# Kernel optimization log

Measured on AMD Instinct MI355X. Metric: run time of the kernel, lower is better.

## Reference

```python
import jax, jax.numpy as jnp
import numpy as np

N_NODES = 100000
N_EDGES = 1600000
N_GRAPHS = 100
HEADS = 8
OUT_CH = 16
IN_FEAT = 128
EPS = 1e-5
NEG_SLOPE = 0.2


def setup_inputs() -> dict:
    key = jax.random.key(0)
    ks = jax.random.split(key, 8)
    x = jax.random.normal(ks[0], (N_NODES, IN_FEAT), dtype=jnp.float32)
    edge_index = jax.random.randint(ks[1], (2, N_EDGES), 0, N_NODES, dtype=jnp.int64)
    batch = jnp.sort(jax.random.randint(ks[2], (N_NODES,), 0, N_GRAPHS, dtype=jnp.int64))
    bn_gamma = jnp.ones((IN_FEAT,), jnp.float32)
    bn_beta = jnp.zeros((IN_FEAT,), jnp.float32)
    W = jax.random.normal(ks[3], (IN_FEAT, HEADS * OUT_CH), dtype=jnp.float32) * (1.0 / np.sqrt(IN_FEAT))
    att_src = jax.random.normal(ks[4], (HEADS, OUT_CH), dtype=jnp.float32) * 0.1
    att_dst = jax.random.normal(ks[5], (HEADS, OUT_CH), dtype=jnp.float32) * 0.1
    bias = jnp.zeros((OUT_CH,), jnp.float32)
    return {"x": x, "edge_index": edge_index, "batch": batch,
            "bn_gamma": bn_gamma, "bn_beta": bn_beta, "W": W,
            "att_src": att_src, "att_dst": att_dst, "bias": bias}


def reference(x, edge_index, batch, bn_gamma, bn_beta, W, att_src, att_dst, bias):
    N = x.shape[0]
    # BatchNorm1d (training mode: batch statistics, biased variance)
    mean = jnp.mean(x, axis=0)
    var = jnp.var(x, axis=0)
    xn = (x - mean) * jax.lax.rsqrt(var + EPS) * bn_gamma + bn_beta

    # GATConv (heads=HEADS, concat=False), with self-loops as in PyG default
    loop = jnp.arange(N, dtype=edge_index.dtype)
    src = jnp.concatenate([edge_index[0], loop])  # [Et]
    dst = jnp.concatenate([edge_index[1], loop])  # [Et]

    h = (xn @ W).reshape(N, HEADS, OUT_CH)  # [N,H,C]
    a_src = jnp.einsum('nhc,hc->nh', h, att_src)  # [N,H]
    a_dst = jnp.einsum('nhc,hc->nh', h, att_dst)  # [N,H]

    e = a_src[src] + a_dst[dst]  # [Et,H]
    e = jnp.where(e > 0, e, NEG_SLOPE * e)  # leaky_relu(0.2)
    # scatter-softmax over destination node (self-loops => every segment nonempty)
    m = jax.ops.segment_max(e, dst, num_segments=N)  # [N,H]
    e = jnp.exp(e - m[dst])
    s = jax.ops.segment_sum(e, dst, num_segments=N)  # [N,H]
    alpha = e / s[dst]  # [Et,H]

    msg = alpha[:, :, None] * h[src]  # [Et,H,C]
    out = jax.ops.segment_sum(msg, dst, num_segments=N)  # [N,H,C]
    out = out.mean(axis=1) + bias  # concat=False -> head mean, [N,C]

    out = jax.nn.elu(out)

    # global_mean_pool over graph ids
    sums = jax.ops.segment_sum(out, batch, num_segments=N_GRAPHS)  # [G,C]
    cnt = jax.ops.segment_sum(jnp.ones((N,), out.dtype), batch, num_segments=N_GRAPHS)
    return sums / jnp.maximum(cnt, 1.0)[:, None]
```

## Files before the change

kernel.cpp:

```cpp
#include <hip/hip_runtime.h>
#include <hip/hip_bf16.h>
#include <hip/hip_fp16.h>


#define N_NODES 100000
#define N_EDGE  1600000
#define N_ET    1700000
#define N_G     100
#define HEADS   8
#define OUTC    16
#define EPS     1e-5f
#define NEG     0.2f
#define NB_BUCKETS 196
#define BCAP    9472
#define EPB     3321

typedef unsigned int uint;
typedef unsigned short ushort;
typedef float f32x2 __attribute__((ext_vector_type(2)));
typedef float f32x4 __attribute__((ext_vector_type(4)));
typedef __bf16 bf16x8 __attribute__((ext_vector_type(8)));

__device__ __forceinline__ float bf2f_lo(uint u){ union{uint i; float f;} c; c.i = u << 16; return c.f; }
__device__ __forceinline__ float bf2f_hi(uint u){ union{uint i; float f;} c; c.i = u & 0xffff0000u; return c.f; }
__device__ __forceinline__ float bf2f(ushort u){ union{uint i; float f;} c; c.i = ((uint)u) << 16; return c.f; }
__device__ __forceinline__ float scrub(float v){ return (v == v) ? v : 0.f; }

__device__ __forceinline__ ushort f2bf(float f){
  union{float ff; uint u;} c; c.ff = f;
  uint u = c.u;
  if ((u & 0x7fffffffu) > 0x7f800000u) u = 0;
  return (ushort)((u + 0x7fffu + ((u >> 16) & 1u)) >> 16);
}
__device__ __forceinline__ ushort bfsan(ushort u){
  return ((ushort)(u & 0x7fffu) > (ushort)0x7f80u) ? (ushort)0 : u;
}

__device__ __forceinline__ float ldf(const void* p, int i, int f32){
  return f32 ? ((const float*)p)[i] : bf2f(((const ushort*)p)[i]);
}
__device__ __forceinline__ int ldid(const int* p, int flat, int is64){
  return is64 ? p[2 * flat] : p[flat];
}

__global__ __launch_bounds__(256) void k_front(const void* __restrict__ xraw,
                                               float* __restrict__ stats,
                                               const int* __restrict__ ei,
                                               int* __restrict__ bcnt,
                                               uint* __restrict__ pairBuf){
  int t = threadIdx.x;
  if (blockIdx.x < 512){
    __shared__ int cdet;
    __shared__ float red[4][256];
    if (t == 0) cdet = 0;
    __syncthreads();
    { uint w = ((const uint*)xraw)[t]; uint el = (w >> 7) & 0xffu;
      if (el != 0 && (el < 110 || el > 140)) atomicAdd(&cdet, 1); }
    __syncthreads();
    int f32 = cdet > 64;
    int c = t & 63;
    int c0 = c * 2;
    float s0 = 0.f, s1 = 0.f, q0 = 0.f, q1 = 0.f;
    if (f32){
      const float2* x2 = (const float2*)xraw;
      for (int r = blockIdx.x * 4 + (t >> 6); r < N_NODES; r += 2048){
        float2 v = x2[r * 64 + c];
        float f0 = scrub(v.x), f1 = scrub(v.y);
        s0 += f0; q0 += f0 * f0;
        s1 += f1; q1 += f1 * f1;
      }
    } else {
      const uint* x2 = (const uint*)xraw;
      for (int r = blockIdx.x * 4 + (t >> 6); r < N_NODES; r += 2048){
        uint v = x2[r * 64 + c];
        float f0 = scrub(bf2f_lo(v)), f1 = scrub(bf2f_hi(v));
        s0 += f0; q0 += f0 * f0;
        s1 += f1; q1 += f1 * f1;
      }
    }
    red[0][t] = s0; red[1][t] = q0; red[2][t] = s1; red[3][t] = q1;
    __syncthreads();
    if (t < 64){
      s0 = red[0][t] + red[0][t+64] + red[0][t+128] + red[0][t+192];
      q0 = red[1][t] + red[1][t+64] + red[1][t+128] + red[1][t+192];
      s1 = red[2][t] + red[2][t+64] + red[2][t+128] + red[2][t+192];
      q1 = red[3][t] + red[3][t+64] + red[3][t+128] + red[3][t+192];
      atomicAdd(&stats[c0],       s0);
      atomicAdd(&stats[c0+1],     s1);
      atomicAdd(&stats[128+c0],   q0);
      atomicAdd(&stats[128+c0+1], q1);
    }
  } else {
    __shared__ int hist[NB_BUCKETS];
    __shared__ int base[NB_BUCKETS];
    __shared__ int cdet2;
    int bid = blockIdx.x - 512;
    if (t == 0) cdet2 = 0;
    for (int i = t; i < NB_BUCKETS; i += 256) hist[i] = 0;
    __syncthreads();
    if (t < 128){ if (ei[2 * t + 1] != 0) atomicAdd(&cdet2, 1); }
    __syncthreads();
    int is64 = cdet2 < 32;
    int e0 = bid * EPB, e1 = min(e0 + EPB, N_ET);
    for (int e = e0 + t; e < e1; e += 256){
      int d = (e < N_EDGE) ? ldid(ei, N_EDGE + e, is64) : (e - N_EDGE);
      uint b = (uint)d >> 9; if (b >= NB_BUCKETS) b = NB_BUCKETS - 1;
      atomicAdd(&hist[b], 1);
    }
    __syncthreads();
    for (int i = t; i < NB_BUCKETS; i += 256){
      int c = hist[i];
      base[i] = c ? atomicAdd(&bcnt[i], c) : 0;
      hist[i] = 0;
    }
    __syncthreads();
    for (int e = e0 + t; e < e1; e += 256){
      int s, d;
      if (e < N_EDGE){ s = ldid(ei, e, is64); d = ldid(ei, N_EDGE + e, is64); }
      else { s = d = e - N_EDGE; }
      uint b = (uint)d >> 9; if (b >= NB_BUCKETS) b = NB_BUCKETS - 1;
      int pos = base[b] + atomicAdd(&hist[b], 1);
      if ((uint)pos < BCAP) pairBuf[(size_t)b * BCAP + pos] = ((uint)s << 9) | ((uint)d & 511u);
    }
  }
}

__global__ __launch_bounds__(128) void k_prep(const float* __restrict__ stats,
                                              const void* __restrict__ gamma,
                                              const void* __restrict__ beta,
                                              const void* __restrict__ W,
                                              const uint* __restrict__ x32,
                                              const int* __restrict__ b32,
                                              ushort* __restrict__ Wpb,
                                              float* __restrict__ bp,
                                              int* __restrict__ flags){
  __shared__ int cnt[2];
  __shared__ float scl8[8], shf8[8];
  int t = threadIdx.x, bid = blockIdx.x;
  if (t < 2) cnt[t] = 0;
  __syncthreads();
  { uint w = x32[t];       uint el = (w >> 7) & 0xffu;
    if (el != 0 && (el < 110 || el > 140)) atomicAdd(&cnt[0], 1); }
  { uint w = x32[t + 128]; uint el = (w >> 7) & 0xffu;
    if (el != 0 && (el < 110 || el > 140)) atomicAdd(&cnt[0], 1); }
  if (bid == 0){ if (b32[98001 + 2 * t] != 0) atomicAdd(&cnt[1], 1); }
  __syncthreads();
  int f32 = cnt[0] > 64;
  if (bid == 0 && t == 0){
    flags[0] = f32;
    flags[1] = 0;
    flags[2] = cnt[1] < 32;
    flags[3] = 0;
  }
  if (t < 8){
    int c = bid * 8 + t;
    float mean = scrub(stats[c] * (1.0f / N_NODES));
    float var  = stats[128 + c] * (1.0f / N_NODES) - mean * mean;
    if (!(var > 0.f)) var = 0.f;
    float sc = scrub(ldf(gamma, c, f32)) * rsqrtf(var + EPS);
    sc = scrub(sc);
    scl8[t] = sc;
    shf8[t] = scrub(scrub(ldf(beta, c, f32)) - mean * sc);
  }
  __syncthreads();
  float bacc = 0.f;
#pragma unroll
  for (int j = 0; j < 8; j++){
    int c = bid * 8 + j;
    float w = scrub(ldf(W, c * 128 + t, f32));
    Wpb[t * 128 + (c & 7) + (((c >> 3) ^ (t & 15)) << 3)] = f2bf(scl8[j] * w);
    bacc += shf8[j] * w;
  }
  atomicAdd(&bp[t], scrub(bacc));
}

__global__ __launch_bounds__(256) void k_gemm(const void* __restrict__ xraw,
                                              const ushort* __restrict__ Wpb,
                                              const float* __restrict__ bp,
                                              const void* __restrict__ att_src,
                                              const void* __restrict__ att_dst,
                                              const int* __restrict__ flags,
                                              unsigned char* __restrict__ h8,
                                              __half* __restrict__ a_src16,
                                              __half* __restrict__ a_dst16){
  int f32 = flags[0];
  __shared__ __align__(16) char smem[33792];
  __shared__ float sSL[128], sDL[128], bpL[128];
  int t = threadIdx.x;
  int wv = t >> 6, l = t & 63;
  int row0 = blockIdx.x * 64;
  if (t < 128){
    sSL[t] = scrub(ldf(att_src, t, f32));
    sDL[t] = scrub(ldf(att_dst, t, f32));
    bpL[t] = bp[t];
  }
  {
    const uint4* wsrc = (const uint4*)Wpb;
    uint4* wdst = (uint4*)smem;
#pragma unroll
    for (int i = 0; i < 8; i++)
      wdst[i * 256 + t] = wsrc[i * 256 + t];
  }
  __syncthreads();
  ushort* BsT = (ushort*)smem;

  f32x4 acc[8];
#pragma unroll
  for (int ct = 0; ct < 8; ct++) acc[ct] = (f32x4){0.f, 0.f, 0.f, 0.f};
  int arow = row0 + wv * 16 + (l & 15);
  int cr = min(arow, N_NODES - 1);
  int kg = (l >> 4) * 8;
  union AB { uint4 q; bf16x8 v; ushort u[8]; };
#pragma unroll
  for (int kc = 0; kc < 4; kc++){
    AB a;
    if (f32){
      const float* xr = (const float*)xraw + (size_t)cr * 128 + kc * 32 + kg;
      float4 p0 = *(const float4*)xr;
      float4 p1 = *(const float4*)(xr + 4);
      a.u[0] = f2bf(p0.x); a.u[1] = f2bf(p0.y); a.u[2] = f2bf(p0.z); a.u[3] = f2bf(p0.w);
      a.u[4] = f2bf(p1.x); a.u[5] = f2bf(p1.y); a.u[6] = f2bf(p1.z); a.u[7] = f2bf(p1.w);
    } else {
      const ushort* xr = (const ushort*)xraw + (size_t)cr * 128 + kc * 32 + kg;
      a.q = *(const uint4*)xr;
#pragma unroll
      for (int j = 0; j < 8; j++) a.u[j] = bfsan(a.u[j]);
    }
#pragma unroll
    for (int ct = 0; ct < 8; ct++){
      int c = ct * 16 + (l & 15);
      int kb = kc * 4 + (l >> 4);
      AB bfr;
      bfr.q = *(const uint4*)(BsT + c * 128 + ((kb ^ (c & 15)) << 3));
      acc[ct] = __builtin_amdgcn_mfma_f32_16x16x32_bf16(a.v, bfr.v, acc[ct], 0, 0, 0);
    }
  }
  __syncthreads();
  float* Cs = (float*)smem;
#pragma unroll
  for (int ct = 0; ct < 8; ct++){
#pragma unroll
    for (int ri = 0; ri < 4; ri++)
      Cs[(wv * 16 + (l >> 4) * 4 + ri) * 132 + ct * 16 + (l & 15)] = acc[ct][ri];
  }
  __syncthreads();
  int row = t >> 2, cg = (t & 3) * 32;
  int r = row0 + row;
  if (r < N_NODES){
    float o[32];
#pragma unroll
    for (int i = 0; i < 8; i++){
      float4 v = *(const float4*)(Cs + row * 132 + cg + i * 4);
      o[i*4+0] = v.x; o[i*4+1] = v.y; o[i*4+2] = v.z; o[i*4+3] = v.w;
    }
#pragma unroll
    for (int j = 0; j < 32; j++){
      float v = scrub(o[j] + bpL[cg + j]);
      o[j] = fminf(fmaxf(v, -448.f), 448.f);
    }
    uint w[8];
#pragma unroll
    for (int i = 0; i < 8; i++){
      uint ww = __builtin_amdgcn_cvt_pk_fp8_f32(o[i*4+0], o[i*4+1], 0, false);
      w[i] = __builtin_amdgcn_cvt_pk_fp8_f32(o[i*4+2], o[i*4+3], (int)ww, true);
    }
    unsigned char* po = h8 + (size_t)r * 128 + cg;
    *(uint4*)po        = make_uint4(w[0], w[1], w[2], w[3]);
    *(uint4*)(po + 16) = make_uint4(w[4], w[5], w[6], w[7]);
    float s0 = 0.f, s1 = 0.f, d0 = 0.f, d1 = 0.f;
#pragma unroll
    for (int j = 0; j < 16; j++){
      s0 += o[j]      * sSL[cg + j];      d0 += o[j]      * sDL[cg + j];
      s1 += o[16 + j] * sSL[cg + 16 + j]; d1 += o[16 + j] * sDL[cg + 16 + j];
    }
    int hA = (t & 3) * 2;
    *(__half2*)(a_src16 + (size_t)r * 8 + hA) = __floats2half2_rn(scrub(s0), scrub(s1));
    *(__half2*)(a_dst16 + (size_t)r * 8 + hA) = __floats2half2_rn(scrub(d0), scrub(d1));
  }
}

__global__ __launch_bounds__(1024) void k_binC(const uint* __restrict__ pairBuf,
                                               const int* __restrict__ bcnt,
                                               int* __restrict__ offsets,
                                               int* __restrict__ csr){
  int b = blockIdx.x, t = threadIdx.x;
  __shared__ int sscan[256];
  __shared__ int degL[512];
  __shared__ int offL[512];
  __shared__ int curL[512];
  if (t < 256) sscan[t] = (t < NB_BUCKETS) ? min(bcnt[t], BCAP) : 0;
  if (t < 512) degL[t] = 0;
  __syncthreads();
  for (int off = 1; off < 256; off <<= 1){
    int add = (t < 256 && t >= off) ? sscan[t - off] : 0;
    __syncthreads();
    if (t < 256) sscan[t] += add;
    __syncthreads();
  }
  int gbase = (b == 0) ? 0 : sscan[b - 1];
  if (b == NB_BUCKETS - 1 && t == 0) offsets[N_NODES] = sscan[NB_BUCKETS - 1];
  int cnt = min(bcnt[b], BCAP);
  const uint* run = pairBuf + (size_t)b * BCAP;
  for (int i = t; i < cnt; i += 1024)
    atomicAdd(&degL[run[i] & 511u], 1);
  __syncthreads();
  int v = (t < 512) ? degL[t] : 0;
  if (t < 512) offL[t] = v;
  __syncthreads();
  for (int off = 1; off < 512; off <<= 1){
    int add = (t < 512 && t >= off) ? offL[t - off] : 0;
    __syncthreads();
    if (t < 512) offL[t] += add;
    __syncthreads();
  }
  if (t < 512){
    int excl = offL[t] - v;
    int node = (b << 9) + t;
    if (node < N_NODES) offsets[node] = gbase + excl;
    offL[t] = excl;
    curL[t] = 0;
  }
  __syncthreads();
  for (int i = t; i < cnt; i += 1024){
    uint e = run[i];
    int dl = e & 511u;
    int s  = e >> 9;
    int pos = atomicAdd(&curL[dl], 1);
    csr[gbase + offL[dl] + pos] = s;
  }
}

__global__ __launch_bounds__(256) void k_msg(const int* __restrict__ offsets, const int* __restrict__ csr,
                                             const __half* __restrict__ a_src16, const __half* __restrict__ a_dst16,
                                             const uint* __restrict__ h32, const void* __restrict__ bias,
                                             const int* __restrict__ flags,
                                             float* __restrict__ out_n){
  int f32 = flags[0];
  int t = threadIdx.x;
  int wv = t >> 6, lane = t & 63;
  int half = lane >> 5, li = lane & 31;
  int myh = li >> 2;
  int n = blockIdx.x * 4 + wv;
  int start = offsets[n], end = offsets[n + 1];
  float ad = __half2float(a_dst16[(size_t)n * 8 + myh]);
  const ushort* as16 = (const ushort*)a_src16;
  float acc0 = 0.f, acc1 = 0.f, acc2 = 0.f, acc3 = 0.f, den = 0.f;

#define PAIR(AA, HH)                                                  \
  { float e = __half2float(*(__half*)&(AA)) + ad;                     \
    e = fmaxf(e, NEG * e);                                            \
    float p = __expf(fminf(e, 30.f));                                 \
    f32x2 lo = __builtin_amdgcn_cvt_pk_f32_fp8((int)(HH), false);     \
    f32x2 hi = __builtin_amdgcn_cvt_pk_f32_fp8((int)(HH), true);      \
    den += p; acc0 += p * lo[0]; acc1 += p * lo[1];                   \
    acc2 += p * hi[0]; acc3 += p * hi[1]; }

  for (int base = start; base < end; base += 64){
    int cnt = min(64, end - base);
    int sreg = csr[min(base + lane, N_ET - 1)];
    int npair = cnt >> 1;
    int jj = 0;
    for (; jj + 4 <= npair; jj += 4){
      int i0 = 2 * jj + half;
      int s0 = __shfl(sreg, i0);
      int s1 = __shfl(sreg, i0 + 2);
      int s2 = __shfl(sreg, i0 + 4);
      int s3 = __shfl(sreg, i0 + 6);
      uint h0 = h32[(uint)s0 * 32u + li];
      uint h1 = h32[(uint)s1 * 32u + li];
      uint h2 = h32[(uint)s2 * 32u + li];
      uint h3 = h32[(uint)s3 * 32u + li];
      ushort a0 = as16[(uint)s0 * 8u + myh];
      ushort a1 = as16[(uint)s1 * 8u + myh];
      ushort a2 = as16[(uint)s2 * 8u + myh];
      ushort a3 = as16[(uint)s3 * 8u + myh];
      __builtin_amdgcn_sched_barrier(0);
      PAIR(a0, h0) PAIR(a1, h1) PAIR(a2, h2) PAIR(a3, h3)
    }
    for (; jj < npair; jj++){
      int s0 = __shfl(sreg, 2 * jj + half);
      uint h0 = h32[(uint)s0 * 32u + li];
      ushort a0 = as16[(uint)s0 * 8u + myh];
      PAIR(a0, h0)
    }
    if (cnt & 1){
      int sl = __shfl(sreg, cnt - 1);
      uint hh = h32[(uint)sl * 32u + li];
      ushort aa = as16[(uint)sl * 8u + myh];
      float e = __half2float(*(__half*)&aa) + ad;
      e = fmaxf(e, NEG * e);
      float p = __expf(fminf(e, 30.f));
      p = half ? 0.f : p;
      f32x2 lo = __builtin_amdgcn_cvt_pk_f32_fp8((int)hh, false);
      f32x2 hi = __builtin_amdgcn_cvt_pk_f32_fp8((int)hh, true);
      den += p; acc0 += p * lo[0]; acc1 += p * lo[1];
      acc2 += p * hi[0]; acc3 += p * hi[1];
    }
  }
#undef PAIR

  den  += __shfl_xor(den, 32);
  acc0 += __shfl_xor(acc0, 32);
  acc1 += __shfl_xor(acc1, 32);
  acc2 += __shfl_xor(acc2, 32);
  acc3 += __shfl_xor(acc3, 32);
  float inv = (den > 0.f) ? (1.0f / den) : 0.f;
  float v0 = acc0 * inv, v1 = acc1 * inv, v2 = acc2 * inv, v3 = acc3 * inv;
  v0 += __shfl_xor(v0, 4);  v1 += __shfl_xor(v1, 4);  v2 += __shfl_xor(v2, 4);  v3 += __shfl_xor(v3, 4);
  v0 += __shfl_xor(v0, 8);  v1 += __shfl_xor(v1, 8);  v2 += __shfl_xor(v2, 8);  v3 += __shfl_xor(v3, 8);
  v0 += __shfl_xor(v0, 16); v1 += __shfl_xor(v1, 16); v2 += __shfl_xor(v2, 16); v3 += __shfl_xor(v3, 16);
  if (lane < 4){
    int c0 = lane * 4;
    float o0 = v0 * 0.125f + scrub(ldf(bias, c0 + 0, f32));
    float o1 = v1 * 0.125f + scrub(ldf(bias, c0 + 1, f32));
    float o2 = v2 * 0.125f + scrub(ldf(bias, c0 + 2, f32));
    float o3 = v3 * 0.125f + scrub(ldf(bias, c0 + 3, f32));
    o0 = o0 > 0.f ? o0 : (__expf(o0) - 1.0f);
    o1 = o1 > 0.f ? o1 : (__expf(o1) - 1.0f);
    o2 = o2 > 0.f ? o2 : (__expf(o2) - 1.0f);
    o3 = o3 > 0.f ? o3 : (__expf(o3) - 1.0f);
    float4* po = (float4*)(out_n + (size_t)n * 16 + c0);
    *po = make_float4(scrub(o0), scrub(o1), scrub(o2), scrub(o3));
  }
}

__global__ __launch_bounds__(256) void k_pool(const float* __restrict__ out_n,
                                              const int* __restrict__ batch,
                                              const int* __restrict__ flags,
                                              float* __restrict__ out){
  int b64 = flags[2];
  int g = blockIdx.x;
  int t = threadIdx.x;
  int c = t & 15, rg = t >> 4;
  int lo = 0, hi = N_NODES;
  while (lo < hi){ int m = (lo + hi) >> 1; if (ldid(batch, m, b64) < g) lo = m + 1; else hi = m; }
  int lo2 = lo, hi2 = N_NODES;
  while (lo2 < hi2){ int m = (lo2 + hi2) >> 1; if (ldid(batch, m, b64) < g + 1) lo2 = m + 1; else hi2 = m; }
  float acc = 0.f;
  for (int r = lo + rg; r < lo2; r += 16)
    acc += out_n[(size_t)r * 16 + c];
  __shared__ float red[16][17];
  red[rg][c] = acc;
  __syncthreads();
  if (t < 16){
    float v = 0.f;
#pragma unroll
    for (int i = 0; i < 16; i++) v += red[i][t];
    float cntf = (float)(lo2 - lo);
    out[g * 16 + t] = scrub(v / fmaxf(cntf, 1.0f));
  }
}

extern "C" void kernel_launch(void* const* d_in, const int* in_sizes, int n_in,
                              void* d_out, int out_size, void* d_ws, size_t ws_size,
                              hipStream_t stream){
  (void)in_sizes; (void)n_in; (void)out_size; (void)ws_size;
  const void* x     = d_in[0];
  const int*  ei    = (const int*)d_in[1];
  const int*  batch = (const int*)d_in[2];
  const void* gamma = d_in[3];
  const void* beta  = d_in[4];
  const void* W     = d_in[5];
  const void* att_s = d_in[6];
  const void* att_d = d_in[7];
  const void* bias  = d_in[8];

  char* ws = (char*)d_ws;
  size_t off = 0;
  auto alloc = [&](size_t b){ size_t r = off; off += (b + 255) & ~(size_t)255; return r; };
  int*    flags   = (int*)(ws + alloc(4 * 4));
  float*  stats   = (float*)(ws + alloc(256 * 4));
  float*  bp      = (float*)(ws + alloc(128 * 4));
  int*    bcnt    = (int*)(ws + alloc(NB_BUCKETS * 4));
  size_t  zero_end = off;
  ushort* Wpb     = (ushort*)(ws + alloc(16384 * 2));
  int*    offsets = (int*)(ws + alloc((size_t)(N_NODES + 1) * 4));
  __half* a_src16 = (__half*)(ws + alloc((size_t)N_NODES * 8 * 2));
  __half* a_dst16 = (__half*)(ws + alloc((size_t)N_NODES * 8 * 2));
  size_t  pb_bytes = (size_t)NB_BUCKETS * BCAP * 4;
  size_t  on_bytes = (size_t)N_NODES * 16 * 4;
  char*   pb_region = ws + alloc(pb_bytes > on_bytes ? pb_bytes : on_bytes);
  uint*   pairBuf = (uint*)pb_region;
  float*  out_n   = (float*)pb_region;
  unsigned char* h8 = (unsigned char*)(ws + alloc((size_t)N_NODES * 128));
  int*    csr     = (int*)(ws + alloc((size_t)N_ET * 4));

  hipMemsetAsync(ws, 0, zero_end, stream);

  k_front<<<1024, 256, 0, stream>>>(x, stats, ei, bcnt, pairBuf);
  k_prep<<<16, 128, 0, stream>>>(stats, gamma, beta, W, (const uint*)x, batch, Wpb, bp, flags);
  k_gemm<<<(N_NODES + 63) / 64, 256, 0, stream>>>(x, Wpb, bp, att_s, att_d, flags, h8, a_src16, a_dst16);
  k_binC<<<NB_BUCKETS, 1024, 0, stream>>>(pairBuf, bcnt, offsets, csr);
  k_msg<<<N_NODES / 4, 256, 0, stream>>>(offsets, csr, a_src16, a_dst16, (const uint*)h8, bias, flags, out_n);
  k_pool<<<N_G, 256, 0, stream>>>(out_n, batch, flags, (float*)d_out);
}
```

Baseline: 279.0 us.

## Fuse prep and CSR build kernels, use finer buckets, cache edges in LDS

Merges the BN/weight prep kernel and the per-bucket CSR build into one launch (k_mid). Destination buckets shrink from 512 to 256 nodes, giving more, smaller bucket blocks. The edge-binning blocks now read each edge once and keep the packed pair and bucket id in shared memory for the scatter pass, instead of re-reading edge_index. The split between stats blocks and binning blocks is rebalanced. This cuts one kernel launch and some global reads, at the cost of more LDS per block and 512-thread blocks in the fused kernel.

```diff
diff --git a/kernel.cpp b/kernel.cpp
--- a/kernel.cpp
+++ b/kernel.cpp
@@ -11,9 +11,11 @@
 #define OUTC    16
 #define EPS     1e-5f
 #define NEG     0.2f
-#define NB_BUCKETS 196
-#define BCAP    9472
-#define EPB     3321
+#define NB_BUCKETS 391
+#define BCAP    4864
+#define BNB     384
+#define ABB     640
+#define EPB     2657
 
 typedef unsigned int uint;
 typedef unsigned short ushort;
@@ -49,7 +51,7 @@
                                                int* __restrict__ bcnt,
                                                uint* __restrict__ pairBuf){
   int t = threadIdx.x;
-  if (blockIdx.x < 512){
+  if (blockIdx.x < BNB){
     __shared__ int cdet;
     __shared__ float red[4][256];
     if (t == 0) cdet = 0;
@@ -63,7 +65,7 @@
     float s0 = 0.f, s1 = 0.f, q0 = 0.f, q1 = 0.f;
     if (f32){
       const float2* x2 = (const float2*)xraw;
-      for (int r = blockIdx.x * 4 + (t >> 6); r < N_NODES; r += 2048){
+      for (int r = blockIdx.x * 4 + (t >> 6); r < N_NODES; r += BNB * 4){
         float2 v = x2[r * 64 + c];
         float f0 = scrub(v.x), f1 = scrub(v.y);
         s0 += f0; q0 += f0 * f0;
@@ -71,7 +73,7 @@
       }
     } else {
       const uint* x2 = (const uint*)xraw;
-      for (int r = blockIdx.x * 4 + (t >> 6); r < N_NODES; r += 2048){
+      for (int r = blockIdx.x * 4 + (t >> 6); r < N_NODES; r += BNB * 4){
         uint v = x2[r * 64 + c];
         float f0 = scrub(bf2f_lo(v)), f1 = scrub(bf2f_hi(v));
         s0 += f0; q0 += f0 * f0;
@@ -93,8 +95,10 @@
   } else {
     __shared__ int hist[NB_BUCKETS];
     __shared__ int base[NB_BUCKETS];
+    __shared__ uint   ebuf[EPB];
+    __shared__ ushort bktL[EPB];
     __shared__ int cdet2;
-    int bid = blockIdx.x - 512;
+    int bid = blockIdx.x - BNB;
     if (t == 0) cdet2 = 0;
     for (int i = t; i < NB_BUCKETS; i += 256) hist[i] = 0;
     __syncthreads();
@@ -103,9 +107,15 @@
     int is64 = cdet2 < 32;
     int e0 = bid * EPB, e1 = min(e0 + EPB, N_ET);
     for (int e = e0 + t; e < e1; e += 256){
-      int d = (e < N_EDGE) ? ldid(ei, N_EDGE + e, is64) : (e - N_EDGE);
-      uint b = (uint)d >> 9; if (b >= NB_BUCKETS) b = NB_BUCKETS - 1;
+      int s, d;
+      if (e < N_EDGE){ s = ldid(ei, e, is64); d = ldid(ei, N_EDGE + e, is64); }
+      else { s = d = e - N_EDGE; }
+      uint dd = (uint)d; if (dd >= N_NODES) dd = 0;
+      uint ss = (uint)s; if (ss >= N_NODES) ss = 0;
+      uint b = dd >> 8;
       atomicAdd(&hist[b], 1);
+      ebuf[e - e0] = (ss << 8) | (dd & 255u);
+      bktL[e - e0] = (ushort)b;
     }
     __syncthreads();
     for (int i = t; i < NB_BUCKETS; i += 256){
@@ -114,64 +124,119 @@
       hist[i] = 0;
     }
     __syncthreads();
-    for (int e = e0 + t; e < e1; e += 256){
-      int s, d;
-      if (e < N_EDGE){ s = ldid(ei, e, is64); d = ldid(ei, N_EDGE + e, is64); }
-      else { s = d = e - N_EDGE; }
-      uint b = (uint)d >> 9; if (b >= NB_BUCKETS) b = NB_BUCKETS - 1;
+    int n_e = e1 - e0;
+    for (int j = t; j < n_e; j += 256){
+      uint b = bktL[j];
       int pos = base[b] + atomicAdd(&hist[b], 1);
-      if ((uint)pos < BCAP) pairBuf[(size_t)b * BCAP + pos] = ((uint)s << 9) | ((uint)d & 511u);
-    }
-  }
-}
-
-__global__ __launch_bounds__(128) void k_prep(const float* __restrict__ stats,
-                                              const void* __restrict__ gamma,
-                                              const void* __restrict__ beta,
-                                              const void* __restrict__ W,
-                                              const uint* __restrict__ x32,
-                                              const int* __restrict__ b32,
-                                              ushort* __restrict__ Wpb,
-                                              float* __restrict__ bp,
-                                              int* __restrict__ flags){
-  __shared__ int cnt[2];
-  __shared__ float scl8[8], shf8[8];
-  int t = threadIdx.x, bid = blockIdx.x;
-  if (t < 2) cnt[t] = 0;
-  __syncthreads();
-  { uint w = x32[t];       uint el = (w >> 7) & 0xffu;
-    if (el != 0 && (el < 110 || el > 140)) atomicAdd(&cnt[0], 1); }
-  { uint w = x32[t + 128]; uint el = (w >> 7) & 0xffu;
-    if (el != 0 && (el < 110 || el > 140)) atomicAdd(&cnt[0], 1); }
-  if (bid == 0){ if (b32[98001 + 2 * t] != 0) atomicAdd(&cnt[1], 1); }
-  __syncthreads();
-  int f32 = cnt[0] > 64;
-  if (bid == 0 && t == 0){
-    flags[0] = f32;
-    flags[1] = 0;
-    flags[2] = cnt[1] < 32;
-    flags[3] = 0;
-  }
-  if (t < 8){
-    int c = bid * 8 + t;
-    float mean = scrub(stats[c] * (1.0f / N_NODES));
-    float var  = stats[128 + c] * (1.0f / N_NODES) - mean * mean;
-    if (!(var > 0.f)) var = 0.f;
-    float sc = scrub(ldf(gamma, c, f32)) * rsqrtf(var + EPS);
-    sc = scrub(sc);
-    scl8[t] = sc;
-    shf8[t] = scrub(scrub(ldf(beta, c, f32)) - mean * sc);
-  }
-  __syncthreads();
-  float bacc = 0.f;
-#pragma unroll
-  for (int j = 0; j < 8; j++){
-    int c = bid * 8 + j;
-    float w = scrub(ldf(W, c * 128 + t, f32));
-    Wpb[t * 128 + (c & 7) + (((c >> 3) ^ (t & 15)) << 3)] = f2bf(scl8[j] * w);
-    bacc += shf8[j] * w;
-  }
-  atomicAdd(&bp[t], scrub(bacc));
+      if ((uint)pos < BCAP) pairBuf[(size_t)b * BCAP + pos] = ebuf[j];
+    }
+  }
+}
+
+__global__ __launch_bounds__(512) void k_mid(const float* __restrict__ stats,
+                                             const void* __restrict__ gamma,
+                                             const void* __restrict__ beta,
+                                             const void* __restrict__ W,
+                                             const uint* __restrict__ x32,
+                                             const int* __restrict__ b32,
+                                             ushort* __restrict__ Wpb,
+                                             float* __restrict__ bp,
+                                             int* __restrict__ flags,
+                                             const uint* __restrict__ pairBuf,
+                                             const int* __restrict__ bcnt,
+                                             int* __restrict__ offsets,
+                                             int* __restrict__ csr){
+  int t = threadIdx.x;
+  if (blockIdx.x < 16){
+    __shared__ int cnt2[2];
+    __shared__ float scl8[8], shf8[8];
+    int bid = blockIdx.x;
+    if (t < 2) cnt2[t] = 0;
+    __syncthreads();
+    if (t < 128){
+      { uint w = x32[t];       uint el = (w >> 7) & 0xffu;
+        if (el != 0 && (el < 110 || el > 140)) atomicAdd(&cnt2[0], 1); }
+      { uint w = x32[t + 128]; uint el = (w >> 7) & 0xffu;
+        if (el != 0 && (el < 110 || el > 140)) atomicAdd(&cnt2[0], 1); }
+      if (bid == 0){ if (b32[98001 + 2 * t] != 0) atomicAdd(&cnt2[1], 1); }
+    }
+    __syncthreads();
+    int f32 = cnt2[0] > 64;
+    if (bid == 0 && t == 0){
+      flags[0] = f32;
+      flags[1] = 0;
+      flags[2] = cnt2[1] < 32;
+      flags[3] = 0;
+    }
+    if (t < 8){
+      int c = bid * 8 + t;
+      float mean = scrub(stats[c] * (1.0f / N_NODES));
+      float var  = stats[128 + c] * (1.0f / N_NODES) - mean * mean;
+      if (!(var > 0.f)) var = 0.f;
+      float sc = scrub(ldf(gamma, c, f32)) * rsqrtf(var + EPS);
+      sc = scrub(sc);
+      scl8[t] = sc;
+      shf8[t] = scrub(scrub(ldf(beta, c, f32)) - mean * sc);
+    }
+    __syncthreads();
+    if (t < 128){
+      float bacc = 0.f;
+#pragma unroll
+      for (int j = 0; j < 8; j++){
+        int c = bid * 8 + j;
+        float w = scrub(ldf(W, c * 128 + t, f32));
+        Wpb[t * 128 + (c & 7) + (((c >> 3) ^ (t & 15)) << 3)] = f2bf(scl8[j] * w);
+        bacc += shf8[j] * w;
+      }
+      atomicAdd(&bp[t], scrub(bacc));
+    }
+  } else {
+    __shared__ int sscan[512];
+    __shared__ int degL[256];
+    __shared__ int offL[256];
+    __shared__ int curL[256];
+    int b = blockIdx.x - 16;
+    sscan[t] = (t < NB_BUCKETS) ? min(bcnt[t], BCAP) : 0;
+    if (t < 256) degL[t] = 0;
+    __syncthreads();
+    for (int off = 1; off < 512; off <<= 1){
+      int add = (t >= off) ? sscan[t - off] : 0;
+      __syncthreads();
+      sscan[t] += add;
+      __syncthreads();
+    }
+    int gbase = (b == 0) ? 0 : sscan[b - 1];
+    if (b == NB_BUCKETS - 1 && t == 0) offsets[N_NODES] = sscan[NB_BUCKETS - 1];
+    int cnt = min(bcnt[b], BCAP);
+    const uint* run = pairBuf + (size_t)b * BCAP;
+    for (int i = t; i < cnt; i += 512)
+      atomicAdd(&degL[run[i] & 255u], 1);
+    __syncthreads();
+    int v = (t < 256) ? degL[t] : 0;
+    if (t < 256) offL[t] = v;
+    __syncthreads();
+    for (int off = 1; off < 256; off <<= 1){
+      int add = (t < 256 && t >= off) ? offL[t - off] : 0;
+      __syncthreads();
+      if (t < 256) offL[t] += add;
+      __syncthreads();
+    }
+    if (t < 256){
+      int excl = offL[t] - v;
+      int node = (b << 8) + t;
+      if (node < N_NODES) offsets[node] = gbase + excl;
+      offL[t] = excl;
+      curL[t] = 0;
+    }
+    __syncthreads();
+    for (int i = t; i < cnt; i += 512){
+      uint e = run[i];
+      int dl = e & 255u;
+      int s  = e >> 8;
+      int pos = atomicAdd(&curL[dl], 1);
+      csr[gbase + offL[dl] + pos] = s;
+    }
+  }
 }
 
 __global__ __launch_bounds__(256) void k_gemm(const void* __restrict__ xraw,
@@ -276,57 +341,6 @@
     int hA = (t & 3) * 2;
     *(__half2*)(a_src16 + (size_t)r * 8 + hA) = __floats2half2_rn(scrub(s0), scrub(s1));
     *(__half2*)(a_dst16 + (size_t)r * 8 + hA) = __floats2half2_rn(scrub(d0), scrub(d1));
-  }
-}
-
-__global__ __launch_bounds__(1024) void k_binC(const uint* __restrict__ pairBuf,
-                                               const int* __restrict__ bcnt,
-                                               int* __restrict__ offsets,
-                                               int* __restrict__ csr){
-  int b = blockIdx.x, t = threadIdx.x;
-  __shared__ int sscan[256];
-  __shared__ int degL[512];
-  __shared__ int offL[512];
-  __shared__ int curL[512];
-  if (t < 256) sscan[t] = (t < NB_BUCKETS) ? min(bcnt[t], BCAP) : 0;
-  if (t < 512) degL[t] = 0;
-  __syncthreads();
-  for (int off = 1; off < 256; off <<= 1){
-    int add = (t < 256 && t >= off) ? sscan[t - off] : 0;
-    __syncthreads();
-    if (t < 256) sscan[t] += add;
-    __syncthreads();
-  }
-  int gbase = (b == 0) ? 0 : sscan[b - 1];
-  if (b == NB_BUCKETS - 1 && t == 0) offsets[N_NODES] = sscan[NB_BUCKETS - 1];
-  int cnt = min(bcnt[b], BCAP);
-  const uint* run = pairBuf + (size_t)b * BCAP;
-  for (int i = t; i < cnt; i += 1024)
-    atomicAdd(&degL[run[i] & 511u], 1);
-  __syncthreads();
-  int v = (t < 512) ? degL[t] : 0;
-  if (t < 512) offL[t] = v;
-  __syncthreads();
-  for (int off = 1; off < 512; off <<= 1){
-    int add = (t < 512 && t >= off) ? offL[t - off] : 0;
-    __syncthreads();
-    if (t < 512) offL[t] += add;
-    __syncthreads();
-  }
-  if (t < 512){
-    int excl = offL[t] - v;
-    int node = (b << 9) + t;
-    if (node < N_NODES) offsets[node] = gbase + excl;
-    offL[t] = excl;
-    curL[t] = 0;
-  }
-  __syncthreads();
-  for (int i = t; i < cnt; i += 1024){
-    uint e = run[i];
-    int dl = e & 511u;
-    int s  = e >> 9;
-    int pos = atomicAdd(&curL[dl], 1);
-    csr[gbase + offL[dl] + pos] = s;
   }
 }
 
@@ -487,10 +501,10 @@
 
   hipMemsetAsync(ws, 0, zero_end, stream);
 
-  k_front<<<1024, 256, 0, stream>>>(x, stats, ei, bcnt, pairBuf);
-  k_prep<<<16, 128, 0, stream>>>(stats, gamma, beta, W, (const uint*)x, batch, Wpb, bp, flags);
+  k_front<<<BNB + ABB, 256, 0, stream>>>(x, stats, ei, bcnt, pairBuf);
+  k_mid<<<16 + NB_BUCKETS, 512, 0, stream>>>(stats, gamma, beta, W, (const uint*)x, batch,
+                                             Wpb, bp, flags, pairBuf, bcnt, offsets, csr);
   k_gemm<<<(N_NODES + 63) / 64, 256, 0, stream>>>(x, Wpb, bp, att_s, att_d, flags, h8, a_src16, a_dst16);
-  k_binC<<<NB_BUCKETS, 1024, 0, stream>>>(pairBuf, bcnt, offsets, csr);
   k_msg<<<N_NODES / 4, 256, 0, stream>>>(offsets, csr, a_src16, a_dst16, (const uint*)h8, bias, flags, out_n);
   k_pool<<<N_G, 256, 0, stream>>>(out_n, batch, flags, (float*)d_out);
 }
```

New measurement: 271.9 us. 2.5% less time.
